# Kernel tuning notes

Hardware: AMD Instinct MI355X
Metric: run time of the kernel (lower is better)

## Reference

```python
import jax, jax.numpy as jnp
import numpy as np
from jax import lax

EPS = 1e-5

def silu(x):
    return x * jax.nn.sigmoid(x)

def setup_inputs() -> dict:
    key = jax.random.key(0)
    ks = jax.random.split(key, 8)
    B, T, H, W = 8, 32, 128, 128
    x = jax.random.normal(ks[0], (B, 1, T, H, W), jnp.float32)
    w_spatial = jax.random.normal(ks[1], (3, 1, 3, 3), jnp.float32) * 0.3
    b_spatial = jax.random.normal(ks[2], (3,), jnp.float32) * 0.1
    w_temporal = jax.random.normal(ks[3], (3, 1, 7, 1), jnp.float32) * 0.3
    b_temporal = jax.random.normal(ks[4], (3,), jnp.float32) * 0.1
    sn_weight = jnp.ones((1, 3, 1, 1, 1), jnp.float32)
    sn_bias = jnp.zeros((1, 3, 1, 1, 1), jnp.float32)
    mean_weight = jnp.ones((3,), jnp.float32)
    var_weight = jnp.ones((3,), jnp.float32)
    w_kv_s = jax.random.normal(ks[5], (2, T), jnp.float32) * (1.0 / np.sqrt(T))
    w_kv_t = jax.random.normal(ks[6], (2, H * W), jnp.float32) * (1.0 / np.sqrt(H * W))
    return dict(x=x, w_spatial=w_spatial, b_spatial=b_spatial,
                w_temporal=w_temporal, b_temporal=b_temporal,
                sn_weight=sn_weight, sn_bias=sn_bias,
                mean_weight=mean_weight, var_weight=var_weight,
                w_kv_s=w_kv_s, w_kv_t=w_kv_t)

def reference(x, w_spatial, b_spatial, w_temporal, b_temporal,
              sn_weight, sn_bias, mean_weight, var_weight, w_kv_s, w_kv_t):
    b, _, t, h, w = x.shape
    C = 3
    # --- spatial cone: timeIsHidden -> Conv2d(1,3,3,pad=1) -> SiLU ---
    xs = x.transpose(0, 2, 1, 3, 4).reshape(b * t, 1, h, w)  # (b t) c h w
    y = lax.conv_general_dilated(xs, w_spatial, (1, 1), ((1, 1), (1, 1)))
    y = silu(y + b_spatial[None, :, None, None])
    y = y.reshape(b, t, C, h, w).transpose(0, 2, 1, 3, 4)  # [b,3,t,h,w]
    # --- temporal cone: spaceIsHidden -> depthwise Conv2d(3,3,(7,1),groups=3) -> SiLU ---
    # kernel is (7,1) so convolving [b,3,t,hw] along t with width-1 in hw is identical math
    yt = y.reshape(b, C, t, h * w)
    z = lax.conv_general_dilated(yt, w_temporal, (1, 1), ((3, 3), (0, 0)),
                                 feature_group_count=C)
    z = silu(z + b_temporal[None, :, None, None]).reshape(b, C, t, h, w)
    # --- gain stage 1: SiLU + SwitchNorm3d(3) (training-mode statistics) ---
    g = silu(z)
    xr = g.reshape(b, C, -1)
    mean_in = xr.mean(-1, keepdims=True)              # [b,C,1] instance stats
    var_in = xr.var(-1, ddof=1, keepdims=True)        # torch .var is unbiased
    temp = var_in + mean_in ** 2
    mean_ln = mean_in.mean(1, keepdims=True)          # layer stats
    var_ln = temp.mean(1, keepdims=True) - mean_ln ** 2
    mean_bn = mean_in.mean(0, keepdims=True)          # batch stats
    var_bn = temp.mean(0, keepdims=True) - mean_bn ** 2
    mw = jax.nn.softmax(mean_weight)
    vw = jax.nn.softmax(var_weight)
    mean = mw[0] * mean_in + mw[1] * mean_ln + mw[2] * mean_bn
    var = vw[0] * var_in + vw[1] * var_ln + vw[2] * var_bn
    xn = ((xr - mean) / jnp.sqrt(var + EPS)).reshape(b, C, t, h, w)
    xn = xn * sn_weight + sn_bias
    # --- gain stage 2: GainControl (spatial/temporal kv via 1x1 convs) ---
    hw = h * w
    # to_kv_spatial: Conv2d(t,2,1,bias=False) over time-as-channel == contraction over t
    kv_s = jnp.einsum('bcthw,ot->bcohw', xn, w_kv_s)   # [b,C,2,h,w]
    ks_ = jax.nn.softmax(kv_s[:, :, 0].reshape(b, C, hw), axis=-1)[:, :, None, :]
    vs_ = kv_s[:, :, 1].reshape(b, C, hw)[:, :, None, :]
    # to_kv_temporal: Conv2d(hw,2,1,bias=False) over space-as-channel == contraction over hw
    xflat = xn.reshape(b, C, t, hw)
    kv_t = jnp.einsum('bcts,os->bcot', xflat, w_kv_t)  # [b,C,2,t]
    kt_ = jax.nn.softmax(kv_t[:, :, 0], axis=-1)[..., None]
    vt_ = kv_t[:, :, 1][..., None]
    out = jnp.sqrt(kt_ * ks_) * (vt_ * vs_)            # [b,C,t,hw]
    return out.reshape(b, C, t, h, w)
```

## Files before the change

### kernel.cpp

```cpp
#include <hip/hip_runtime.h>
#include <hip/hip_bf16.h>
#include <hip/hip_fp16.h>

#define Bn 8
#define Cn 3
#define Tn 32
#define Hn 128
#define Wn 128
#define HWn (Hn * Wn)
#define Nn (Tn * HWn)
#define EPSn 1e-5f
#define QT 4
#define SCH 128
#define SSW (SCH * QT)

__device__ __forceinline__ float silu_f(float v) {
    return v * __builtin_amdgcn_rcpf(1.0f + __expf(-v));
}

__global__ __launch_bounds__(256) void k1_spatial(
    const float* __restrict__ x, const float* __restrict__ wsp,
    const float* __restrict__ bsp, __half* __restrict__ y)
{
    const int tid = threadIdx.x;
    const int sub = tid & 31;
    const int bt = blockIdx.x;
    const int b = bt >> 5, t = bt & 31;
    const int row = blockIdx.y * 8 + (tid >> 5);
    const int col = sub * 4;

    float w[27], bb[3];
#pragma unroll
    for (int i = 0; i < 27; ++i) w[i] = wsp[i];
#pragma unroll
    for (int i = 0; i < 3; ++i) bb[i] = bsp[i];

    const float* xsl = x + ((size_t)b * Tn + t) * HWn + (size_t)row * Wn + col;
    const bool upok = row > 0, dnok = row < Hn - 1;
    const float4 z4 = make_float4(0.f, 0.f, 0.f, 0.f);
    float4 xm = upok ? *(const float4*)(xsl - Wn) : z4;
    float4 xc = *(const float4*)(xsl);
    float4 xp = dnok ? *(const float4*)(xsl + Wn) : z4;
    float xv[3][6];
    {
        float lu, rd;
        lu = __shfl_up(xm.w, 1);  rd = __shfl_down(xm.x, 1);
        xv[0][0] = (sub == 0) ? 0.f : lu; xv[0][1] = xm.x; xv[0][2] = xm.y;
        xv[0][3] = xm.z; xv[0][4] = xm.w; xv[0][5] = (sub == 31) ? 0.f : rd;
        lu = __shfl_up(xc.w, 1);  rd = __shfl_down(xc.x, 1);
        xv[1][0] = (sub == 0) ? 0.f : lu; xv[1][1] = xc.x; xv[1][2] = xc.y;
        xv[1][3] = xc.z; xv[1][4] = xc.w; xv[1][5] = (sub == 31) ? 0.f : rd;
        lu = __shfl_up(xp.w, 1);  rd = __shfl_down(xp.x, 1);
        xv[2][0] = (sub == 0) ? 0.f : lu; xv[2][1] = xp.x; xv[2][2] = xp.y;
        xv[2][3] = xp.z; xv[2][4] = xp.w; xv[2][5] = (sub == 31) ? 0.f : rd;
    }
#pragma unroll
    for (int c = 0; c < 3; ++c) {
        float s0 = bb[c], s1 = bb[c], s2 = bb[c], s3 = bb[c];
#pragma unroll
        for (int i = 0; i < 3; ++i) {
#pragma unroll
            for (int j = 0; j < 3; ++j) {
                const float wv = w[c * 9 + i * 3 + j];
                s0 += wv * xv[i][j];
                s1 += wv * xv[i][j + 1];
                s2 += wv * xv[i][j + 2];
                s3 += wv * xv[i][j + 3];
            }
        }
        __half2 o01 = __floats2half2_rn(silu_f(s0), silu_f(s1));
        __half2 o23 = __floats2half2_rn(silu_f(s2), silu_f(s3));
        __half2* dst = (__half2*)(y + ((size_t)(b * 3 + c) * Tn + t) * HWn
                                  + (size_t)row * Wn + col);
        dst[0] = o01; dst[1] = o23;
    }
}

template<int QTg>
__device__ __forceinline__ void k2_body(
    const __half* __restrict__ y, const float* __restrict__ wtp,
    const float* __restrict__ btp, const float* __restrict__ wkt,
    const float* __restrict__ wks,
    __half* __restrict__ raw0, __half* __restrict__ raw1,
    float* __restrict__ pt0p, float* __restrict__ pt1p,
    float* __restrict__ ss0p, float* __restrict__ ss1p)
{
    constexpr int O0 = QTg * 8;
    constexpr int O1 = O0 + 8;
    constexpr int SLO = (O0 - 3 < 0) ? 0 : (O0 - 3);
    constexpr int SHI = (O1 + 2 > Tn - 1) ? (Tn - 1) : (O1 + 2);

    const int tid = threadIdx.x, lane = tid & 63, wave = tid >> 6;
    const int sch = blockIdx.x * 4 + wave;
    const int bc  = blockIdx.y;
    const int c = bc % 3;
    const int s0i = sch * 128 + lane * 2;

    __half2 wt_h[7];
#pragma unroll
    for (int i = 0; i < 7; ++i) {
        const float wv = wtp[c * 7 + i];
        wt_h[i] = __floats2half2_rn(wv, wv);
    }
    const float bt_f = btp[c];
    const __half2 bt_h = __floats2half2_rn(bt_f, bt_f);

    const __half* yb = y + (size_t)bc * Nn + s0i;
    const float2 k0v = *(const float2*)(wkt + s0i);
    const float2 k1v = *(const float2*)(wkt + HWn + s0i);

    __half2 ring[7];
    float2 a0 = make_float2(0.f, 0.f), a1 = make_float2(0.f, 0.f);
    float ps = 0.f, pq = 0.f;
    float pt0a[8], pt1a[8];

#pragma unroll
    for (int tt = SLO; tt <= SHI + 3; ++tt) {
        if (tt <= SHI) {
            ring[tt % 7] = *(const __half2*)(yb + (size_t)tt * HWn);
        }
        const int to = tt - 3;
        if (to >= O0 && to < O1) {
            __half2 acc = bt_h;
#pragma unroll
            for (int k = 0; k < 7; ++k) {
                const int ts = to + k - 3;
                if (ts >= 0 && ts < Tn)
                    acc = __hfma2(wt_h[k], ring[ts % 7], acc);
            }
            const float2 tv = __half22float2(acc);
            const float g0 = silu_f(silu_f(tv.x));
            const float g1 = silu_f(silu_f(tv.y));
            const float wk0 = wks[to];
            const float wk1 = wks[Tn + to];
            a0.x += wk0 * g0; a0.y += wk0 * g1;
            a1.x += wk1 * g0; a1.y += wk1 * g1;
            ps += g0 + g1;
            pq += g0 * g0 + g1 * g1;
            pt0a[to - O0] = k0v.x * g0 + k0v.y * g1;
            pt1a[to - O0] = k1v.x * g0 + k1v.y * g1;
        }
    }

#pragma unroll
    for (int i = 0; i < 8; ++i) {
        pt0a[i] += __shfl_xor(pt0a[i], 1, 64);
        pt0a[i] += __shfl_xor(pt0a[i], 2, 64);
        pt0a[i] += __shfl_xor(pt0a[i], 4, 64);
        pt1a[i] += __shfl_xor(pt1a[i], 1, 64);
        pt1a[i] += __shfl_xor(pt1a[i], 2, 64);
        pt1a[i] += __shfl_xor(pt1a[i], 4, 64);
    }
    {
        const int j = lane & 7;
        float r0 = (j == 0) ? pt0a[0] : (j == 1) ? pt0a[1] : (j == 2) ? pt0a[2]
                 : (j == 3) ? pt0a[3] : (j == 4) ? pt0a[4] : (j == 5) ? pt0a[5]
                 : (j == 6) ? pt0a[6] : pt0a[7];
        float r1 = (j == 0) ? pt1a[0] : (j == 1) ? pt1a[1] : (j == 2) ? pt1a[2]
                 : (j == 3) ? pt1a[3] : (j == 4) ? pt1a[4] : (j == 5) ? pt1a[5]
                 : (j == 6) ? pt1a[6] : pt1a[7];
        r0 += __shfl_xor(r0, 8, 64); r0 += __shfl_xor(r0, 16, 64); r0 += __shfl_xor(r0, 32, 64);
        r1 += __shfl_xor(r1, 8, 64); r1 += __shfl_xor(r1, 16, 64); r1 += __shfl_xor(r1, 32, 64);
        if (lane < 8)
            pt0p[((size_t)bc * Tn + O0 + lane) * SCH + sch] = r0;
        else if (lane < 16)
            pt1p[((size_t)bc * Tn + O0 + (lane & 7)) * SCH + sch] = r1;
    }
    {
        float p0 = ps, p1 = pq;
        p0 += __shfl_xor(p0, 1, 64); p0 += __shfl_xor(p0, 2, 64); p0 += __shfl_xor(p0, 4, 64);
        p1 += __shfl_xor(p1, 1, 64); p1 += __shfl_xor(p1, 2, 64); p1 += __shfl_xor(p1, 4, 64);
        float r = (lane & 1) ? p1 : p0;
        r += __shfl_xor(r, 8, 64);
        r += __shfl_xor(r, 16, 64);
        r += __shfl_xor(r, 32, 64);
        if (lane == 0) ss0p[(size_t)bc * SSW + sch * QT + QTg] = r;
        if (lane == 1) ss1p[(size_t)bc * SSW + sch * QT + QTg] = r;
    }
    {
        const size_t off = (size_t)(QTg * 24 + bc) * HWn + s0i;
        *(__half2*)(raw0 + off) = __floats2half2_rn(a0.x, a0.y);
        *(__half2*)(raw1 + off) = __floats2half2_rn(a1.x, a1.y);
    }
}

__global__ __launch_bounds__(256) void k2_temporal(
    const __half* __restrict__ y, const float* __restrict__ wtp,
    const float* __restrict__ btp, const float* __restrict__ wkt,
    const float* __restrict__ wks,
    __half* __restrict__ raw0, __half* __restrict__ raw1,
    float* __restrict__ pt0p, float* __restrict__ pt1p,
    float* __restrict__ ss0p, float* __restrict__ ss1p)
{
    switch (blockIdx.z) {
    case 0: k2_body<0>(y, wtp, btp, wkt, wks, raw0, raw1, pt0p, pt1p, ss0p, ss1p); break;
    case 1: k2_body<1>(y, wtp, btp, wkt, wks, raw0, raw1, pt0p, pt1p, ss0p, ss1p); break;
    case 2: k2_body<2>(y, wtp, btp, wkt, wks, raw0, raw1, pt0p, pt1p, ss0p, ss1p); break;
    default: k2_body<3>(y, wtp, btp, wkt, wks, raw0, raw1, pt0p, pt1p, ss0p, ss1p); break;
    }
}

__global__ __launch_bounds__(256) void k3a_reduce(
    const float* __restrict__ pt0p, const float* __restrict__ pt1p,
    const float* __restrict__ ss0p, const float* __restrict__ ss1p,
    const float* __restrict__ wkt, const float* __restrict__ wks,
    const __half* __restrict__ raw0, const __half* __restrict__ raw1,
    float* __restrict__ kvt0r, float* __restrict__ kvt1r,
    float* __restrict__ ssS, float* __restrict__ ssSS, float* __restrict__ wsum,
    __half* __restrict__ v0s, __half* __restrict__ v1s)
{
    const int blk = blockIdx.x;
    const int tid = threadIdx.x;
    if (blk < Bn * Cn) {
        const int t = tid >> 3, g = tid & 7;
        const float4* p0 = (const float4*)(pt0p + ((size_t)blk * Tn + t) * SCH) + g * 4;
        const float4* p1 = (const float4*)(pt1p + ((size_t)blk * Tn + t) * SCH) + g * 4;
        float4 A0 = p0[0], A1 = p0[1], A2 = p0[2], A3 = p0[3];
        float4 B0 = p1[0], B1 = p1[1], B2 = p1[2], B3 = p1[3];
        float s0 = ((A0.x + A0.y) + (A0.z + A0.w)) + ((A1.x + A1.y) + (A1.z + A1.w))
                 + ((A2.x + A2.y) + (A2.z + A2.w)) + ((A3.x + A3.y) + (A3.z + A3.w));
        float s1 = ((B0.x + B0.y) + (B0.z + B0.w)) + ((B1.x + B1.y) + (B1.z + B1.w))
                 + ((B2.x + B2.y) + (B2.z + B2.w)) + ((B3.x + B3.y) + (B3.z + B3.w));
        s0 += __shfl_xor(s0, 1, 64); s0 += __shfl_xor(s0, 2, 64); s0 += __shfl_xor(s0, 4, 64);
        s1 += __shfl_xor(s1, 1, 64); s1 += __shfl_xor(s1, 2, 64); s1 += __shfl_xor(s1, 4, 64);
        if (g == 0) { kvt0r[blk * Tn + t] = s0; kvt1r[blk * Tn + t] = s1; }
        const float4* q0 = (const float4*)(ss0p + (size_t)blk * SSW);
        const float4* q1 = (const float4*)(ss1p + (size_t)blk * SSW);
        float a = 0.f, bb = 0.f;
        if (tid < SSW / 4) {
            float4 a4 = q0[tid], b4 = q1[tid];
            a = (a4.x + a4.y) + (a4.z + a4.w);
            bb = (b4.x + b4.y) + (b4.z + b4.w);
        }
        __shared__ float r0[256], r1[256];
        r0[tid] = a; r1[tid] = bb;
        __syncthreads();
        for (int off = 128; off > 0; off >>= 1) {
            if (tid < off) { r0[tid] += r0[tid + off]; r1[tid] += r1[tid + off]; }
            __syncthreads();
        }
        if (tid == 0) { ssS[blk] = r0[0]; ssSS[blk] = r1[0]; }
    } else if (blk == Bn * Cn) {
        const float4* w0 = (const float4*)wkt;
        const float4* w1 = (const float4*)(wkt + HWn);
        float l0 = 0.f, l1 = 0.f;
        for (int i = tid; i < HWn / 4; i += 256) {
            float4 t0 = w0[i], t1 = w1[i];
            l0 += (t0.x + t0.y) + (t0.z + t0.w);
            l1 += (t1.x + t1.y) + (t1.z + t1.w);
        }
        __shared__ float r0[256], r1[256];
        r0[tid] = l0; r1[tid] = l1;
        __syncthreads();
        for (int off = 128; off > 0; off >>= 1) {
            if (tid < off) { r0[tid] += r0[tid + off]; r1[tid] += r1[tid + off]; }
            __syncthreads();
        }
        if (tid == 0) { wsum[0] = r0[0]; wsum[1] = r1[0]; }
        if (tid < 64) {
            float v = wks[tid];
            v += __shfl_xor(v, 1, 64); v += __shfl_xor(v, 2, 64);
            v += __shfl_xor(v, 4, 64); v += __shfl_xor(v, 8, 64);
            v += __shfl_xor(v, 16, 64);
            if (tid == 0) wsum[2] = v;
            if (tid == 32) wsum[3] = v;
        }
    } else {
        const int rs = blk - (Bn * Cn + 1);
        const int bc = rs >> 3, sl = rs & 7;
        const size_t idx = (size_t)bc * HWn + sl * 2048 + tid * 8;
        float acc0[8] = {0,0,0,0,0,0,0,0}, acc1[8] = {0,0,0,0,0,0,0,0};
#pragma unroll
        for (int q = 0; q < QT; ++q) {
            float4 h0 = *(const float4*)(raw0 + (size_t)q * 24 * HWn + idx);
            float4 h1 = *(const float4*)(raw1 + (size_t)q * 24 * HWn + idx);
            const __half2* p0 = (const __half2*)&h0;
            const __half2* p1 = (const __half2*)&h1;
#pragma unroll
            for (int j = 0; j < 4; ++j) {
                float2 f0 = __half22float2(p0[j]);
                float2 f1 = __half22float2(p1[j]);
                acc0[j * 2] += f0.x; acc0[j * 2 + 1] += f0.y;
                acc1[j * 2] += f1.x; acc1[j * 2 + 1] += f1.y;
            }
        }
        float4 o0, o1;
        __half2* s0 = (__half2*)&o0; __half2* s1 = (__half2*)&o1;
#pragma unroll
        for (int j = 0; j < 4; ++j) {
            s0[j] = __floats2half2_rn(acc0[j * 2], acc0[j * 2 + 1]);
            s1[j] = __floats2half2_rn(acc1[j * 2], acc1[j * 2 + 1]);
        }
        *(float4*)(v0s + idx) = o0;
        *(float4*)(v1s + idx) = o1;
    }
}

__global__ __launch_bounds__(256) void k6_fused(
    const __half* __restrict__ v0s, const __half* __restrict__ v1s,
    const float* __restrict__ kvt0r, const float* __restrict__ kvt1r,
    const float* __restrict__ ssS, const float* __restrict__ ssSS,
    const float* __restrict__ wsum, const float* __restrict__ mean_w,
    const float* __restrict__ var_w, const float* __restrict__ snw,
    const float* __restrict__ snb, float* __restrict__ out)
{
    const int ch = blockIdx.x;
    const int bc = blockIdx.y;
    const int tid = threadIdx.x, lane = tid & 63, wave = tid >> 6;
    const int b = bc / 3, c = bc % 3;
    const float Nf = (float)Nn;

    float mln = 0.f, tln = 0.f;
#pragma unroll
    for (int cc = 0; cc < 3; ++cc) {
        float S = ssS[b * 3 + cc], SS = ssSS[b * 3 + cc];
        float m = S / Nf;
        float v = (SS - S * m) / (Nf - 1.0f);
        mln += m; tln += v + m * m;
    }
    mln *= (1.0f / 3.0f); tln *= (1.0f / 3.0f);
    const float vln = tln - mln * mln;
    float mbn = 0.f, tbn = 0.f;
#pragma unroll
    for (int bb2 = 0; bb2 < 8; ++bb2) {
        float S = ssS[bb2 * 3 + c], SS = ssSS[bb2 * 3 + c];
        float m = S / Nf;
        float v = (SS - S * m) / (Nf - 1.0f);
        mbn += m; tbn += v + m * m;
    }
    mbn *= 0.125f; tbn *= 0.125f;
    const float vbn = tbn - mbn * mbn;
    const float S_own = ssS[bc], SS_own = ssSS[bc];
    const float mean_in = S_own / Nf;
    const float var_in = (SS_own - S_own * mean_in) / (Nf - 1.0f);
    float mw0, mw1, mw2, vw0, vw1, vw2;
    {
        float m0 = mean_w[0], m1 = mean_w[1], m2 = mean_w[2];
        float mm = fmaxf(m0, fmaxf(m1, m2));
        float e0 = __expf(m0 - mm), e1 = __expf(m1 - mm), e2 = __expf(m2 - mm);
        float inv = 1.0f / (e0 + e1 + e2);
        mw0 = e0 * inv; mw1 = e1 * inv; mw2 = e2 * inv;
    }
    {
        float v0 = var_w[0], v1 = var_w[1], v2 = var_w[2];
        float vm = fmaxf(v0, fmaxf(v1, v2));
        float e0 = __expf(v0 - vm), e1 = __expf(v1 - vm), e2 = __expf(v2 - vm);
        float inv = 1.0f / (e0 + e1 + e2);
        vw0 = e0 * inv; vw1 = e1 * inv; vw2 = e2 * inv;
    }
    const float mean = mw0 * mean_in + mw1 * mln + mw2 * mbn;
    const float var  = vw0 * var_in + vw1 * vln + vw2 * vbn;
    const float sc = snw[c] / sqrtf(var + EPSn);
    const float sf = snb[c] - mean * sc;
    const float c0 = sf * wsum[2], c1 = sf * wsum[3];
    const float Wt0 = wsum[0], Wt1 = wsum[1];

    __shared__ float aSh[Tn];
    if (tid < Tn) {
        float k0 = sc * kvt0r[bc * Tn + tid] + sf * Wt0;
        float k1 = sc * kvt1r[bc * Tn + tid] + sf * Wt1;
        float m = k0;
#pragma unroll
        for (int d = 1; d < 32; d <<= 1) m = fmaxf(m, __shfl_xor(m, d, 64));
        float e = __expf(k0 - m);
        float s = e;
#pragma unroll
        for (int d = 1; d < 32; d <<= 1) s += __shfl_xor(s, d, 64);
        aSh[tid] = sqrtf(e / s) * k1;
    }

    const __half* p0a = v0s + (size_t)bc * HWn;
    float m_run = -3.4e38f, s_run = 0.f;
#pragma unroll
    for (int i = 0; i < 8; ++i) {
        const int idx = tid * 8 + i * 2048;
        float4 hv = *(const float4*)(p0a + idx);
        const __half2* hp = (const __half2*)&hv;
        float vals[8];
#pragma unroll
        for (int j = 0; j < 4; ++j) {
            float2 f = __half22float2(hp[j]);
            vals[j * 2] = sc * f.x + c0;
            vals[j * 2 + 1] = sc * f.y + c0;
        }
        float vm = vals[0];
#pragma unroll
        for (int j = 1; j < 8; ++j) vm = fmaxf(vm, vals[j]);
        const float mn = fmaxf(m_run, vm);
        float sl = 0.f;
#pragma unroll
        for (int j = 0; j < 8; ++j) sl += __expf(vals[j] - mn);
        s_run = s_run * __expf(m_run - mn) + sl;
        m_run = mn;
    }
#pragma unroll
    for (int d = 1; d < 64; d <<= 1) {
        const float mo = __shfl_xor(m_run, d, 64);
        const float so = __shfl_xor(s_run, d, 64);
        const float mn = fmaxf(m_run, mo);
        s_run = s_run * __expf(m_run - mn) + so * __expf(mo - mn);
        m_run = mn;
    }
    __shared__ float wm[4], wsv[4];
    if (lane == 0) { wm[wave] = m_run; wsv[wave] = s_run; }
    __syncthreads();
    float M = fmaxf(fmaxf(wm[0], wm[1]), fmaxf(wm[2], wm[3]));
    float Sexp = wsv[0] * __expf(wm[0] - M) + wsv[1] * __expf(wm[1] - M)
               + wsv[2] * __expf(wm[2] - M) + wsv[3] * __expf(wm[3] - M);
    const float invS = __builtin_amdgcn_rcpf(Sexp);

    const int s = ch * 1024 + tid * 4;
    float2 h0 = *(const float2*)(p0a + s);
    float2 h1 = *(const float2*)(v1s + (size_t)bc * HWn + s);
    const __half2* q0 = (const __half2*)&h0;
    const __half2* q1 = (const __half2*)&h1;
    float2 u0l = __half22float2(q0[0]), u0h = __half22float2(q0[1]);
    float2 u1l = __half22float2(q1[0]), u1h = __half22float2(q1[1]);
    float4 Bv;
    Bv.x = sqrtf(__expf(sc * u0l.x + c0 - M) * invS) * (sc * u1l.x + c1);
    Bv.y = sqrtf(__expf(sc * u0l.y + c0 - M) * invS) * (sc * u1l.y + c1);
    Bv.z = sqrtf(__expf(sc * u0h.x + c0 - M) * invS) * (sc * u1h.x + c1);
    Bv.w = sqrtf(__expf(sc * u0h.y + c0 - M) * invS) * (sc * u1h.y + c1);
    float* op = out + (size_t)bc * Nn + s;
#pragma unroll
    for (int t = 0; t < Tn; ++t) {
        const float av = aSh[t];
        float4 o; o.x = av * Bv.x; o.y = av * Bv.y; o.z = av * Bv.z; o.w = av * Bv.w;
        *(float4*)(op + (size_t)t * HWn) = o;
    }
}

extern "C" void kernel_launch(void* const* d_in, const int* in_sizes, int n_in,
                              void* d_out, int out_size, void* d_ws, size_t ws_size,
                              hipStream_t stream) {
    const float* x          = (const float*)d_in[0];
    const float* w_spatial  = (const float*)d_in[1];
    const float* b_spatial  = (const float*)d_in[2];
    const float* w_temporal = (const float*)d_in[3];
    const float* b_temporal = (const float*)d_in[4];
    const float* sn_weight  = (const float*)d_in[5];
    const float* sn_bias    = (const float*)d_in[6];
    const float* mean_weight= (const float*)d_in[7];
    const float* var_weight = (const float*)d_in[8];
    const float* w_kv_s     = (const float*)d_in[9];
    const float* w_kv_t     = (const float*)d_in[10];
    float* out = (float*)d_out;
    float* ws  = (float*)d_ws;

    __half* yh   = (__half*)ws;
    __half* raw0 = (__half*)(ws + 6291456);
    __half* raw1 = raw0 + (size_t)QT * Bn * Cn * HWn;
    float* pt0p  = ws + 6291456 + 2 * 786432;
    float* pt1p  = pt0p + (size_t)Bn * Cn * Tn * SCH;
    float* ss0p  = pt1p + (size_t)Bn * Cn * Tn * SCH;
    float* ss1p  = ss0p + (size_t)Bn * Cn * SSW;
    __half* v0s  = (__half*)(ss1p + (size_t)Bn * Cn * SSW);
    __half* v1s  = v0s + (size_t)Bn * Cn * HWn;
    float* kvt0r = (float*)(v1s + (size_t)Bn * Cn * HWn);
    float* kvt1r = kvt0r + Bn * Cn * Tn;
    float* ssS   = kvt1r + Bn * Cn * Tn;
    float* ssSS  = ssS + 24;
    float* wsum  = ssSS + 24;

    k1_spatial<<<dim3(Bn * Tn, Hn / 8), 256, 0, stream>>>(x, w_spatial, b_spatial, yh);
    k2_temporal<<<dim3(SCH / 4, Bn * Cn, QT), 256, 0, stream>>>(yh, w_temporal,
                                                                b_temporal, w_kv_t,
                                                                w_kv_s, raw0, raw1,
                                                                pt0p, pt1p, ss0p, ss1p);
    k3a_reduce<<<Bn * Cn + 1 + 192, 256, 0, stream>>>(pt0p, pt1p, ss0p, ss1p,
                                                      w_kv_t, w_kv_s, raw0, raw1,
                                                      kvt0r, kvt1r, ssS, ssSS, wsum,
                                                      v0s, v1s);
    k6_fused<<<dim3(16, Bn * Cn), 256, 0, stream>>>(v0s, v1s, kvt0r, kvt1r,
                                                    ssS, ssSS, wsum, mean_weight,
                                                    var_weight, sn_weight, sn_bias, out);
}
```

Before: 54.24 us.

## Eliminate reduce kernel by folding its work into spatial and final kernels

Removes the separate k3a_reduce launch. The weight-sum reduction moves into an extra grid row of the spatial kernel. The per-(b,c) statistic and kv_t reductions, plus summing the QT partial raw planes, are now recomputed redundantly inside each block of the final fused kernel. This saves one launch and the v0s/v1s intermediate round-trip, but each of the 384 final blocks re-reads all ss partials and re-reads the raw0 plane set four times.

```diff
diff --git a/kernel.cpp b/kernel.cpp
--- a/kernel.cpp
+++ b/kernel.cpp
@@ -20,9 +20,39 @@
 
 __global__ __launch_bounds__(256) void k1_spatial(
     const float* __restrict__ x, const float* __restrict__ wsp,
-    const float* __restrict__ bsp, __half* __restrict__ y)
+    const float* __restrict__ bsp, const float* __restrict__ wkt,
+    const float* __restrict__ wks, __half* __restrict__ y,
+    float* __restrict__ wsum)
 {
     const int tid = threadIdx.x;
+    if (blockIdx.y == Hn / 8) {
+        if (blockIdx.x != 0) return;
+        __shared__ float r0[256], r1[256];
+        const float4* w0 = (const float4*)wkt;
+        const float4* w1 = (const float4*)(wkt + HWn);
+        float l0 = 0.f, l1 = 0.f;
+        for (int i = tid; i < HWn / 4; i += 256) {
+            float4 t0 = w0[i], t1 = w1[i];
+            l0 += (t0.x + t0.y) + (t0.z + t0.w);
+            l1 += (t1.x + t1.y) + (t1.z + t1.w);
+        }
+        r0[tid] = l0; r1[tid] = l1;
+        __syncthreads();
+        for (int off = 128; off > 0; off >>= 1) {
+            if (tid < off) { r0[tid] += r0[tid + off]; r1[tid] += r1[tid + off]; }
+            __syncthreads();
+        }
+        if (tid == 0) { wsum[0] = r0[0]; wsum[1] = r1[0]; }
+        if (tid < 64) {
+            float v = wks[tid];
+            v += __shfl_xor(v, 1, 64); v += __shfl_xor(v, 2, 64);
+            v += __shfl_xor(v, 4, 64); v += __shfl_xor(v, 8, 64);
+            v += __shfl_xor(v, 16, 64);
+            if (tid == 0) wsum[2] = v;
+            if (tid == 32) wsum[3] = v;
+        }
+        return;
+    }
     const int sub = tid & 31;
     const int bt = blockIdx.x;
     const int b = bt >> 5, t = bt & 31;
@@ -200,106 +230,10 @@
     }
 }
 
-__global__ __launch_bounds__(256) void k3a_reduce(
+__global__ __launch_bounds__(256) void k6_fused(
+    const __half* __restrict__ raw0, const __half* __restrict__ raw1,
     const float* __restrict__ pt0p, const float* __restrict__ pt1p,
     const float* __restrict__ ss0p, const float* __restrict__ ss1p,
-    const float* __restrict__ wkt, const float* __restrict__ wks,
-    const __half* __restrict__ raw0, const __half* __restrict__ raw1,
-    float* __restrict__ kvt0r, float* __restrict__ kvt1r,
-    float* __restrict__ ssS, float* __restrict__ ssSS, float* __restrict__ wsum,
-    __half* __restrict__ v0s, __half* __restrict__ v1s)
-{
-    const int blk = blockIdx.x;
-    const int tid = threadIdx.x;
-    if (blk < Bn * Cn) {
-        const int t = tid >> 3, g = tid & 7;
-        const float4* p0 = (const float4*)(pt0p + ((size_t)blk * Tn + t) * SCH) + g * 4;
-        const float4* p1 = (const float4*)(pt1p + ((size_t)blk * Tn + t) * SCH) + g * 4;
-        float4 A0 = p0[0], A1 = p0[1], A2 = p0[2], A3 = p0[3];
-        float4 B0 = p1[0], B1 = p1[1], B2 = p1[2], B3 = p1[3];
-        float s0 = ((A0.x + A0.y) + (A0.z + A0.w)) + ((A1.x + A1.y) + (A1.z + A1.w))
-                 + ((A2.x + A2.y) + (A2.z + A2.w)) + ((A3.x + A3.y) + (A3.z + A3.w));
-        float s1 = ((B0.x + B0.y) + (B0.z + B0.w)) + ((B1.x + B1.y) + (B1.z + B1.w))
-                 + ((B2.x + B2.y) + (B2.z + B2.w)) + ((B3.x + B3.y) + (B3.z + B3.w));
-        s0 += __shfl_xor(s0, 1, 64); s0 += __shfl_xor(s0, 2, 64); s0 += __shfl_xor(s0, 4, 64);
-        s1 += __shfl_xor(s1, 1, 64); s1 += __shfl_xor(s1, 2, 64); s1 += __shfl_xor(s1, 4, 64);
-        if (g == 0) { kvt0r[blk * Tn + t] = s0; kvt1r[blk * Tn + t] = s1; }
-        const float4* q0 = (const float4*)(ss0p + (size_t)blk * SSW);
-        const float4* q1 = (const float4*)(ss1p + (size_t)blk * SSW);
-        float a = 0.f, bb = 0.f;
-        if (tid < SSW / 4) {
-            float4 a4 = q0[tid], b4 = q1[tid];
-            a = (a4.x + a4.y) + (a4.z + a4.w);
-            bb = (b4.x + b4.y) + (b4.z + b4.w);
-        }
-        __shared__ float r0[256], r1[256];
-        r0[tid] = a; r1[tid] = bb;
-        __syncthreads();
-        for (int off = 128; off > 0; off >>= 1) {
-            if (tid < off) { r0[tid] += r0[tid + off]; r1[tid] += r1[tid + off]; }
-            __syncthreads();
-        }
-        if (tid == 0) { ssS[blk] = r0[0]; ssSS[blk] = r1[0]; }
-    } else if (blk == Bn * Cn) {
-        const float4* w0 = (const float4*)wkt;
-        const float4* w1 = (const float4*)(wkt + HWn);
-        float l0 = 0.f, l1 = 0.f;
-        for (int i = tid; i < HWn / 4; i += 256) {
-            float4 t0 = w0[i], t1 = w1[i];
-            l0 += (t0.x + t0.y) + (t0.z + t0.w);
-            l1 += (t1.x + t1.y) + (t1.z + t1.w);
-        }
-        __shared__ float r0[256], r1[256];
-        r0[tid] = l0; r1[tid] = l1;
-        __syncthreads();
-        for (int off = 128; off > 0; off >>= 1) {
-            if (tid < off) { r0[tid] += r0[tid + off]; r1[tid] += r1[tid + off]; }
-            __syncthreads();
-        }
-        if (tid == 0) { wsum[0] = r0[0]; wsum[1] = r1[0]; }
-        if (tid < 64) {
-            float v = wks[tid];
-            v += __shfl_xor(v, 1, 64); v += __shfl_xor(v, 2, 64);
-            v += __shfl_xor(v, 4, 64); v += __shfl_xor(v, 8, 64);
-            v += __shfl_xor(v, 16, 64);
-            if (tid == 0) wsum[2] = v;
-            if (tid == 32) wsum[3] = v;
-        }
-    } else {
-        const int rs = blk - (Bn * Cn + 1);
-        const int bc = rs >> 3, sl = rs & 7;
-        const size_t idx = (size_t)bc * HWn + sl * 2048 + tid * 8;
-        float acc0[8] = {0,0,0,0,0,0,0,0}, acc1[8] = {0,0,0,0,0,0,0,0};
-#pragma unroll
-        for (int q = 0; q < QT; ++q) {
-            float4 h0 = *(const float4*)(raw0 + (size_t)q * 24 * HWn + idx);
-            float4 h1 = *(const float4*)(raw1 + (size_t)q * 24 * HWn + idx);
-            const __half2* p0 = (const __half2*)&h0;
-            const __half2* p1 = (const __half2*)&h1;
-#pragma unroll
-            for (int j = 0; j < 4; ++j) {
-                float2 f0 = __half22float2(p0[j]);
-                float2 f1 = __half22float2(p1[j]);
-                acc0[j * 2] += f0.x; acc0[j * 2 + 1] += f0.y;
-                acc1[j * 2] += f1.x; acc1[j * 2 + 1] += f1.y;
-            }
-        }
-        float4 o0, o1;
-        __half2* s0 = (__half2*)&o0; __half2* s1 = (__half2*)&o1;
-#pragma unroll
-        for (int j = 0; j < 4; ++j) {
-            s0[j] = __floats2half2_rn(acc0[j * 2], acc0[j * 2 + 1]);
-            s1[j] = __floats2half2_rn(acc1[j * 2], acc1[j * 2 + 1]);
-        }
-        *(float4*)(v0s + idx) = o0;
-        *(float4*)(v1s + idx) = o1;
-    }
-}
-
-__global__ __launch_bounds__(256) void k6_fused(
-    const __half* __restrict__ v0s, const __half* __restrict__ v1s,
-    const float* __restrict__ kvt0r, const float* __restrict__ kvt1r,
-    const float* __restrict__ ssS, const float* __restrict__ ssSS,
     const float* __restrict__ wsum, const float* __restrict__ mean_w,
     const float* __restrict__ var_w, const float* __restrict__ snw,
     const float* __restrict__ snb, float* __restrict__ out)
@@ -310,10 +244,46 @@
     const int b = bc / 3, c = bc % 3;
     const float Nf = (float)Nn;
 
+    __shared__ float ssS_sh[24], ssSS_sh[24];
+    __shared__ float kv0_sh[Tn], kv1_sh[Tn];
+    __shared__ float aSh[Tn];
+    __shared__ float wm[4], wsv[4];
+
+    if (tid < 192) {
+        const int sbc = tid >> 3, part = tid & 7;
+        const float4* q0 = (const float4*)(ss0p + (size_t)sbc * SSW) + part * 16;
+        const float4* q1 = (const float4*)(ss1p + (size_t)sbc * SSW) + part * 16;
+        float a = 0.f, bb = 0.f;
+#pragma unroll
+        for (int j = 0; j < 16; ++j) {
+            float4 t0 = q0[j], t1 = q1[j];
+            a += (t0.x + t0.y) + (t0.z + t0.w);
+            bb += (t1.x + t1.y) + (t1.z + t1.w);
+        }
+        a += __shfl_xor(a, 1, 64); a += __shfl_xor(a, 2, 64); a += __shfl_xor(a, 4, 64);
+        bb += __shfl_xor(bb, 1, 64); bb += __shfl_xor(bb, 2, 64); bb += __shfl_xor(bb, 4, 64);
+        if (part == 0) { ssS_sh[sbc] = a; ssSS_sh[sbc] = bb; }
+    }
+    {
+        const int t = tid >> 3, g = tid & 7;
+        const float4* p0 = (const float4*)(pt0p + ((size_t)bc * Tn + t) * SCH) + g * 4;
+        const float4* p1 = (const float4*)(pt1p + ((size_t)bc * Tn + t) * SCH) + g * 4;
+        float4 A0 = p0[0], A1 = p0[1], A2 = p0[2], A3 = p0[3];
+        float4 B0 = p1[0], B1 = p1[1], B2 = p1[2], B3 = p1[3];
+        float s0 = ((A0.x + A0.y) + (A0.z + A0.w)) + ((A1.x + A1.y) + (A1.z + A1.w))
+                 + ((A2.x + A2.y) + (A2.z + A2.w)) + ((A3.x + A3.y) + (A3.z + A3.w));
+        float s1 = ((B0.x + B0.y) + (B0.z + B0.w)) + ((B1.x + B1.y) + (B1.z + B1.w))
+                 + ((B2.x + B2.y) + (B2.z + B2.w)) + ((B3.x + B3.y) + (B3.z + B3.w));
+        s0 += __shfl_xor(s0, 1, 64); s0 += __shfl_xor(s0, 2, 64); s0 += __shfl_xor(s0, 4, 64);
+        s1 += __shfl_xor(s1, 1, 64); s1 += __shfl_xor(s1, 2, 64); s1 += __shfl_xor(s1, 4, 64);
+        if (g == 0) { kv0_sh[t] = s0; kv1_sh[t] = s1; }
+    }
+    __syncthreads();
+
     float mln = 0.f, tln = 0.f;
 #pragma unroll
     for (int cc = 0; cc < 3; ++cc) {
-        float S = ssS[b * 3 + cc], SS = ssSS[b * 3 + cc];
+        float S = ssS_sh[b * 3 + cc], SS = ssSS_sh[b * 3 + cc];
         float m = S / Nf;
         float v = (SS - S * m) / (Nf - 1.0f);
         mln += m; tln += v + m * m;
@@ -323,14 +293,14 @@
     float mbn = 0.f, tbn = 0.f;
 #pragma unroll
     for (int bb2 = 0; bb2 < 8; ++bb2) {
-        float S = ssS[bb2 * 3 + c], SS = ssSS[bb2 * 3 + c];
+        float S = ssS_sh[bb2 * 3 + c], SS = ssSS_sh[bb2 * 3 + c];
         float m = S / Nf;
         float v = (SS - S * m) / (Nf - 1.0f);
         mbn += m; tbn += v + m * m;
     }
     mbn *= 0.125f; tbn *= 0.125f;
     const float vbn = tbn - mbn * mbn;
-    const float S_own = ssS[bc], SS_own = ssSS[bc];
+    const float S_own = ssS_sh[bc], SS_own = ssSS_sh[bc];
     const float mean_in = S_own / Nf;
     const float var_in = (SS_own - S_own * mean_in) / (Nf - 1.0f);
     float mw0, mw1, mw2, vw0, vw1, vw2;
@@ -355,10 +325,9 @@
     const float c0 = sf * wsum[2], c1 = sf * wsum[3];
     const float Wt0 = wsum[0], Wt1 = wsum[1];
 
-    __shared__ float aSh[Tn];
     if (tid < Tn) {
-        float k0 = sc * kvt0r[bc * Tn + tid] + sf * Wt0;
-        float k1 = sc * kvt1r[bc * Tn + tid] + sf * Wt1;
+        float k0 = sc * kv0_sh[tid] + sf * Wt0;
+        float k1 = sc * kv1_sh[tid] + sf * Wt1;
         float m = k0;
 #pragma unroll
         for (int d = 1; d < 32; d <<= 1) m = fmaxf(m, __shfl_xor(m, d, 64));
@@ -369,20 +338,25 @@
         aSh[tid] = sqrtf(e / s) * k1;
     }
 
-    const __half* p0a = v0s + (size_t)bc * HWn;
+    const __half* r0b = raw0 + (size_t)bc * HWn;
     float m_run = -3.4e38f, s_run = 0.f;
 #pragma unroll
     for (int i = 0; i < 8; ++i) {
         const int idx = tid * 8 + i * 2048;
-        float4 hv = *(const float4*)(p0a + idx);
-        const __half2* hp = (const __half2*)&hv;
+        float acc[8] = {0, 0, 0, 0, 0, 0, 0, 0};
+#pragma unroll
+        for (int q = 0; q < QT; ++q) {
+            float4 hv = *(const float4*)(r0b + (size_t)q * 24 * HWn + idx);
+            const __half2* hp = (const __half2*)&hv;
+#pragma unroll
+            for (int j = 0; j < 4; ++j) {
+                float2 f = __half22float2(hp[j]);
+                acc[j * 2] += f.x; acc[j * 2 + 1] += f.y;
+            }
+        }
         float vals[8];
 #pragma unroll
-        for (int j = 0; j < 4; ++j) {
-            float2 f = __half22float2(hp[j]);
-            vals[j * 2] = sc * f.x + c0;
-            vals[j * 2 + 1] = sc * f.y + c0;
-        }
+        for (int j = 0; j < 8; ++j) vals[j] = sc * acc[j] + c0;
         float vm = vals[0];
 #pragma unroll
         for (int j = 1; j < 8; ++j) vm = fmaxf(vm, vals[j]);
@@ -401,7 +375,6 @@
         s_run = s_run * __expf(m_run - mn) + so * __expf(mo - mn);
         m_run = mn;
     }
-    __shared__ float wm[4], wsv[4];
     if (lane == 0) { wm[wave] = m_run; wsv[wave] = s_run; }
     __syncthreads();
     float M = fmaxf(fmaxf(wm[0], wm[1]), fmaxf(wm[2], wm[3]));
@@ -410,17 +383,24 @@
     const float invS = __builtin_amdgcn_rcpf(Sexp);
 
     const int s = ch * 1024 + tid * 4;
-    float2 h0 = *(const float2*)(p0a + s);
-    float2 h1 = *(const float2*)(v1s + (size_t)bc * HWn + s);
-    const __half2* q0 = (const __half2*)&h0;
-    const __half2* q1 = (const __half2*)&h1;
-    float2 u0l = __half22float2(q0[0]), u0h = __half22float2(q0[1]);
-    float2 u1l = __half22float2(q1[0]), u1h = __half22float2(q1[1]);
+    const __half* r1b = raw1 + (size_t)bc * HWn;
+    float a0[4] = {0, 0, 0, 0}, a1[4] = {0, 0, 0, 0};
+#pragma unroll
+    for (int q = 0; q < QT; ++q) {
+        float2 h0 = *(const float2*)(r0b + (size_t)q * 24 * HWn + s);
+        float2 h1 = *(const float2*)(r1b + (size_t)q * 24 * HWn + s);
+        const __half2* q0 = (const __half2*)&h0;
+        const __half2* q1 = (const __half2*)&h1;
+        float2 f0l = __half22float2(q0[0]), f0h = __half22float2(q0[1]);
+        float2 f1l = __half22float2(q1[0]), f1h = __half22float2(q1[1]);
+        a0[0] += f0l.x; a0[1] += f0l.y; a0[2] += f0h.x; a0[3] += f0h.y;
+        a1[0] += f1l.x; a1[1] += f1l.y; a1[2] += f1h.x; a1[3] += f1h.y;
+    }
     float4 Bv;
-    Bv.x = sqrtf(__expf(sc * u0l.x + c0 - M) * invS) * (sc * u1l.x + c1);
-    Bv.y = sqrtf(__expf(sc * u0l.y + c0 - M) * invS) * (sc * u1l.y + c1);
-    Bv.z = sqrtf(__expf(sc * u0h.x + c0 - M) * invS) * (sc * u1h.x + c1);
-    Bv.w = sqrtf(__expf(sc * u0h.y + c0 - M) * invS) * (sc * u1h.y + c1);
+    Bv.x = sqrtf(__expf(sc * a0[0] + c0 - M) * invS) * (sc * a1[0] + c1);
+    Bv.y = sqrtf(__expf(sc * a0[1] + c0 - M) * invS) * (sc * a1[1] + c1);
+    Bv.z = sqrtf(__expf(sc * a0[2] + c0 - M) * invS) * (sc * a1[2] + c1);
+    Bv.w = sqrtf(__expf(sc * a0[3] + c0 - M) * invS) * (sc * a1[3] + c1);
     float* op = out + (size_t)bc * Nn + s;
 #pragma unroll
     for (int t = 0; t < Tn; ++t) {
@@ -454,24 +434,15 @@
     float* pt1p  = pt0p + (size_t)Bn * Cn * Tn * SCH;
     float* ss0p  = pt1p + (size_t)Bn * Cn * Tn * SCH;
     float* ss1p  = ss0p + (size_t)Bn * Cn * SSW;
-    __half* v0s  = (__half*)(ss1p + (size_t)Bn * Cn * SSW);
-    __half* v1s  = v0s + (size_t)Bn * Cn * HWn;
-    float* kvt0r = (float*)(v1s + (size_t)Bn * Cn * HWn);
-    float* kvt1r = kvt0r + Bn * Cn * Tn;
-    float* ssS   = kvt1r + Bn * Cn * Tn;
-    float* ssSS  = ssS + 24;
-    float* wsum  = ssSS + 24;
-
-    k1_spatial<<<dim3(Bn * Tn, Hn / 8), 256, 0, stream>>>(x, w_spatial, b_spatial, yh);
+    float* wsum  = ss1p + (size_t)Bn * Cn * SSW;
+
+    k1_spatial<<<dim3(Bn * Tn, Hn / 8 + 1), 256, 0, stream>>>(x, w_spatial, b_spatial,
+                                                              w_kv_t, w_kv_s, yh, wsum);
     k2_temporal<<<dim3(SCH / 4, Bn * Cn, QT), 256, 0, stream>>>(yh, w_temporal,
                                                                 b_temporal, w_kv_t,
                                                                 w_kv_s, raw0, raw1,
                                                                 pt0p, pt1p, ss0p, ss1p);
-    k3a_reduce<<<Bn * Cn + 1 + 192, 256, 0, stream>>>(pt0p, pt1p, ss0p, ss1p,
-                                                      w_kv_t, w_kv_s, raw0, raw1,
-                                                      kvt0r, kvt1r, ssS, ssSS, wsum,
-                                                      v0s, v1s);
-    k6_fused<<<dim3(16, Bn * Cn), 256, 0, stream>>>(v0s, v1s, kvt0r, kvt1r,
-                                                    ssS, ssSS, wsum, mean_weight,
+    k6_fused<<<dim3(16, Bn * Cn), 256, 0, stream>>>(raw0, raw1, pt0p, pt1p,
+                                                    ss0p, ss1p, wsum, mean_weight,
                                                     var_weight, sn_weight, sn_bias, out);
 }
```

Result: slower. 57.43 us (+5.9%).
